# Kernel optimization log

Measured on AMD Instinct MI355X. Metric: run time of the kernel, lower is better.

Reference implementation:

```python
import jax, jax.numpy as jnp
import numpy as np

B, E, H, W, L = 16, 32, 512, 512, 3  # batch, emb channels, height, width, n classes (bg/plant/disease)
MAX_NEIGHBOR = 3


def _per_image_loss(emb, pred, label, neighbor):
    """emb: (E,H,W) f32; pred: (L,H,W) f32 logits; label: (H,W) int32; neighbor: (L,MAX_NEIGHBOR) int32."""
    P = H * W
    emb_f = emb.reshape(E, P)                                      # (E,P)
    lab_f = label.reshape(P)
    onehot = (lab_f[None, :] == jnp.arange(L)[:, None]).astype(emb.dtype)  # (L,P)
    counts = onehot.sum(axis=1)                                    # (L,)

    # per-label mean embeddings (segment mean) and L2-normalized means (F.normalize eps=1e-12)
    means = (onehot @ emb_f.T) / counts[:, None]                   # (L,E)
    norm_means = means / jnp.maximum(jnp.linalg.norm(means, axis=1, keepdims=True), 1e-12)

    # intra loss: mean over masked pixels of (1 - cos(norm_mean, pixel)), labels 1..L-1
    pix_hat = emb_f / jnp.maximum(jnp.linalg.norm(emb_f, axis=0, keepdims=True), 1e-8)  # CosineSimilarity eps
    cos = norm_means @ pix_hat                                     # (L,P)
    intra_per = (onehot * (1.0 - cos)).sum(axis=1) / counts        # (L,)
    intra = intra_per[1:].sum() / (L - 1)

    # inter loss: pairwise cosine of normalized means, masked by neighbor table
    S = norm_means @ norm_means.T                                  # (L,L)
    # inter_mask: for main_label>=1, mark neighbor entries until first 0 (break semantics)
    valid = jnp.cumprod((neighbor != 0).astype(jnp.float32), axis=1)        # (L,MAX_NEIGHBOR)
    rows = jnp.broadcast_to(jnp.arange(L)[:, None], (L, MAX_NEIGHBOR))
    row_ok = (rows >= 1).astype(jnp.float32)
    mask = jnp.zeros((L, L), dtype=jnp.float32).at[
        rows.reshape(-1), neighbor.reshape(-1)
    ].max((valid * row_ok).reshape(-1))
    inter = (S * mask).sum() / mask.sum()

    # cross-entropy (labels in [0,L), ignore_index=255 never hit here), mean over pixels
    logp = jax.nn.log_softmax(pred, axis=0)                        # (L,H,W)
    ce = -jnp.take_along_axis(logp, label[None, :, :].astype(jnp.int32), axis=0).mean()

    return intra + inter + ce


def setup_inputs() -> dict:
    key = jax.random.key(0)
    k1, k2, k3 = jax.random.split(key, 3)
    embedding = jax.random.normal(k1, (B, E, H, W), dtype=jnp.float32)
    prediction = jax.random.normal(k2, (B, L, H, W), dtype=jnp.float32)
    class_label = jax.random.randint(k3, (B, H, W), 0, L).astype(jnp.int32)
    # realistic neighbor table: plant(1)<->disease(2) adjacent, 0 = terminator
    nb = np.tile(np.array([[0, 0, 0], [2, 0, 0], [1, 0, 0]], dtype=np.int32), (B, 1, 1))
    neighbor = jnp.asarray(nb)
    return {"embedding": embedding, "prediction": prediction,
            "class_label": class_label, "neighbor": neighbor}


def reference(embedding, prediction, class_label, neighbor):
    losses = jax.vmap(_per_image_loss)(embedding, prediction, class_label, neighbor)  # (B,)
    return losses.sum()
```

## Files before the change

kernel.cpp:

```cpp
#include <hip/hip_runtime.h>
#include <math.h>

#define BATCH 16
#define EMB   32
#define HW    262144
#define NL    3

#define BLOCKS_PER_IMG 128
#define PX_PER_BLOCK  (HW / BLOCKS_PER_IMG)
#define TILE_PX       128
#define N_ITERS       (PX_PER_BLOCK / TILE_PX)

#define WS_COUNTS 0
#define WS_SE     64
#define WS_SH     (WS_SE + BATCH*96)
#define WS_CE     (WS_SH + BATCH*96)
#define WS_FLOATS (WS_CE + 1)

__device__ __forceinline__ float ce1(float a, float b, float c, int l) {
    const float m = fmaxf(fmaxf(a, b), c);
    const float s = __expf(a - m) + __expf(b - m) + __expf(c - m);
    const float zl = (l == 0) ? a : ((l == 1) ? b : c);
    return m + __logf(s) - zl;
}

__global__ __launch_bounds__(256) void fused_kernel(
        const float* __restrict__ emb, const float* __restrict__ pred,
        const int* __restrict__ label, float* __restrict__ ws)
{
    const int tid = threadIdx.x;
    const int ps  = tid & 31;
    const int eg  = tid >> 5;
    const int wv  = tid >> 6;
    const bool lowHalf = (tid & 63) < 32;
    const int b   = blockIdx.x / BLOCKS_PER_IMG;
    const int blk = blockIdx.x % BLOCKS_PER_IMG;

    const float* embB  = emb  + (size_t)b * EMB * HW;
    const float* predB = pred + (size_t)b * 3 * HW;
    const int*   labB  = label + (size_t)b * HW;
    const size_t pixBase = (size_t)blk * PX_PER_BLOCK;

    const float* ch0 = embB + (size_t)(eg*4+0)*HW;
    const float* ch1 = embB + (size_t)(eg*4+1)*HW;
    const float* ch2 = embB + (size_t)(eg*4+2)*HW;
    const float* ch3 = embB + (size_t)(eg*4+3)*HW;

    __shared__ float4 part[2][4][32];

    float accE[NL][4] = {};
    float accH[NL][4] = {};
    float cnt[NL] = {0.f, 0.f, 0.f};
    float ce = 0.f;

    size_t p = pixBase + (size_t)ps * 4;
    float4 v0 = *(const float4*)(ch0 + p);
    float4 v1 = *(const float4*)(ch1 + p);
    float4 v2 = *(const float4*)(ch2 + p);
    float4 v3 = *(const float4*)(ch3 + p);
    int4  lab = *(const int4*)(labB + p);

    for (int it = 0; it < N_ITERS; ++it) {
        const size_t pn = (it + 1 < N_ITERS) ? (p + TILE_PX)
                                             : (pixBase + (size_t)ps * 4);
        const float4 n0 = *(const float4*)(ch0 + pn);
        const float4 n1 = *(const float4*)(ch1 + pn);
        const float4 n2 = *(const float4*)(ch2 + pn);
        const float4 n3 = *(const float4*)(ch3 + pn);
        const int4 nlab = *(const int4*)(labB + pn);

        const bool doCE = (eg == (it & 7));
        float4 z0, z1, z2;
        if (doCE) {
            z0 = *(const float4*)(predB + p);
            z1 = *(const float4*)(predB + HW + p);
            z2 = *(const float4*)(predB + 2*HW + p);
        }

        float4 s;
        s.x = v0.x*v0.x + v1.x*v1.x + v2.x*v2.x + v3.x*v3.x;
        s.y = v0.y*v0.y + v1.y*v1.y + v2.y*v2.y + v3.y*v3.y;
        s.z = v0.z*v0.z + v1.z*v1.z + v2.z*v2.z + v3.z*v3.z;
        s.w = v0.w*v0.w + v1.w*v1.w + v2.w*v2.w + v3.w*v3.w;
        s.x += __shfl_xor(s.x, 32);
        s.y += __shfl_xor(s.y, 32);
        s.z += __shfl_xor(s.z, 32);
        s.w += __shfl_xor(s.w, 32);
        if (lowHalf) part[it & 1][wv][ps] = s;
        __syncthreads();
        const float4 t0 = part[it & 1][0][ps];
        const float4 t1 = part[it & 1][1][ps];
        const float4 t2 = part[it & 1][2][ps];
        const float4 t3 = part[it & 1][3][ps];
        float invn[4];
        invn[0] = 1.0f / fmaxf(sqrtf(t0.x + t1.x + t2.x + t3.x), 1e-8f);
        invn[1] = 1.0f / fmaxf(sqrtf(t0.y + t1.y + t2.y + t3.y), 1e-8f);
        invn[2] = 1.0f / fmaxf(sqrtf(t0.z + t1.z + t2.z + t3.z), 1e-8f);
        invn[3] = 1.0f / fmaxf(sqrtf(t0.w + t1.w + t2.w + t3.w), 1e-8f);

        const float chv[4][4] = {
            {v0.x, v1.x, v2.x, v3.x},
            {v0.y, v1.y, v2.y, v3.y},
            {v0.z, v1.z, v2.z, v3.z},
            {v0.w, v1.w, v2.w, v3.w}};
        const int labs[4] = {lab.x, lab.y, lab.z, lab.w};

        #pragma unroll
        for (int j = 0; j < 4; ++j) {
            const float m0 = (labs[j] == 0) ? 1.f : 0.f;
            const float m1 = (labs[j] == 1) ? 1.f : 0.f;
            const float m2 = (labs[j] == 2) ? 1.f : 0.f;
            const float iv = invn[j];
            if (eg == 0) { cnt[0] += m0; cnt[1] += m1; cnt[2] += m2; }
            #pragma unroll
            for (int k = 0; k < 4; ++k) {
                const float v  = chv[j][k];
                const float vh = v * iv;
                accE[0][k] = fmaf(m0, v,  accE[0][k]);
                accE[1][k] = fmaf(m1, v,  accE[1][k]);
                accE[2][k] = fmaf(m2, v,  accE[2][k]);
                accH[0][k] = fmaf(m0, vh, accH[0][k]);
                accH[1][k] = fmaf(m1, vh, accH[1][k]);
                accH[2][k] = fmaf(m2, vh, accH[2][k]);
            }
        }

        if (doCE) {
            ce += ce1(z0.x, z1.x, z2.x, labs[0]);
            ce += ce1(z0.y, z1.y, z2.y, labs[1]);
            ce += ce1(z0.z, z1.z, z2.z, labs[2]);
            ce += ce1(z0.w, z1.w, z2.w, labs[3]);
        }

        v0 = n0; v1 = n1; v2 = n2; v3 = n3; lab = nlab; p = pn;
    }

    #pragma unroll
    for (int o = 16; o >= 1; o >>= 1) {
        #pragma unroll
        for (int l = 0; l < NL; ++l) {
            #pragma unroll
            for (int k = 0; k < 4; ++k) {
                accE[l][k] += __shfl_xor(accE[l][k], o);
                accH[l][k] += __shfl_xor(accH[l][k], o);
            }
            cnt[l] += __shfl_xor(cnt[l], o);
        }
        ce += __shfl_xor(ce, o);
    }
    if (ps == 0) {
        float* se = ws + WS_SE + b * 96;
        float* sh = ws + WS_SH + b * 96;
        #pragma unroll
        for (int l = 0; l < NL; ++l) {
            #pragma unroll
            for (int k = 0; k < 4; ++k) {
                atomicAdd(&se[l*32 + eg*4 + k], accE[l][k]);
                atomicAdd(&sh[l*32 + eg*4 + k], accH[l][k]);
            }
        }
        atomicAdd(&ws[WS_CE], ce * (1.0f / (float)HW));
        if (eg == 0) {
            atomicAdd(&ws[WS_COUNTS + b*4 + 0], cnt[0]);
            atomicAdd(&ws[WS_COUNTS + b*4 + 1], cnt[1]);
            atomicAdd(&ws[WS_COUNTS + b*4 + 2], cnt[2]);
        }
    }
}

__global__ __launch_bounds__(512) void final_kernel(
        const int* __restrict__ nbr, const float* __restrict__ ws,
        float* __restrict__ out)
{
    const int tid = threadIdx.x;
    const int b = tid >> 5;
    const int e = tid & 31;
    __shared__ float total;
    if (tid == 0) total = 0.f;
    __syncthreads();

    const float* se = ws + WS_SE + b * 96;
    const float* sh = ws + WS_SH + b * 96;
    const float c0 = ws[WS_COUNTS + b*4 + 0];
    const float c1 = ws[WS_COUNTS + b*4 + 1];
    const float c2 = ws[WS_COUNTS + b*4 + 2];

    float mean0 = se[0*32 + e] / c0;
    float mean1 = se[1*32 + e] / c1;
    float mean2 = se[2*32 + e] / c2;

    float n0 = mean0*mean0, n1 = mean1*mean1, n2 = mean2*mean2;
    #pragma unroll
    for (int o = 16; o >= 1; o >>= 1) {
        n0 += __shfl_xor(n0, o);
        n1 += __shfl_xor(n1, o);
        n2 += __shfl_xor(n2, o);
    }
    const float nm0 = mean0 / fmaxf(sqrtf(n0), 1e-12f);
    const float nm1 = mean1 / fmaxf(sqrtf(n1), 1e-12f);
    const float nm2 = mean2 / fmaxf(sqrtf(n2), 1e-12f);

    float d1  = nm1 * sh[1*32 + e];
    float d2  = nm2 * sh[2*32 + e];
    float s10 = nm1 * nm0, s11 = nm1 * nm1, s12 = nm1 * nm2;
    float s20 = nm2 * nm0, s21 = nm2 * nm1, s22 = nm2 * nm2;
    #pragma unroll
    for (int o = 16; o >= 1; o >>= 1) {
        d1  += __shfl_xor(d1, o);  d2  += __shfl_xor(d2, o);
        s10 += __shfl_xor(s10, o); s11 += __shfl_xor(s11, o); s12 += __shfl_xor(s12, o);
        s20 += __shfl_xor(s20, o); s21 += __shfl_xor(s21, o); s22 += __shfl_xor(s22, o);
    }

    if (e == 0) {
        float S[3][3];
        S[1][0] = s10; S[1][1] = s11; S[1][2] = s12;
        S[2][0] = s20; S[2][1] = s21; S[2][2] = s22;
        S[0][0] = S[0][1] = S[0][2] = 0.f;
        float mask[3][3] = {{0.f,0.f,0.f},{0.f,0.f,0.f},{0.f,0.f,0.f}};
        for (int row = 1; row < 3; ++row) {
            int prod = 1;
            for (int j = 0; j < 3; ++j) {
                const int v = nbr[b*9 + row*3 + j];
                if (v == 0) prod = 0;
                if (prod) mask[row][v] = 1.f;
            }
        }
        float num = 0.f, den = 0.f;
        for (int row = 1; row < 3; ++row)
            for (int col = 0; col < 3; ++col) {
                num += S[row][col] * mask[row][col];
                den += mask[row][col];
            }
        const float inter = num / den;
        const float ip1 = 1.f - d1 / c1;
        const float ip2 = 1.f - d2 / c2;
        const float loss = 0.5f * (ip1 + ip2) + inter;
        atomicAdd(&total, loss);
    }
    __syncthreads();
    if (tid == 0) out[0] = total + ws[WS_CE];
}

extern "C" void kernel_launch(void* const* d_in, const int* in_sizes, int n_in,
                              void* d_out, int out_size, void* d_ws, size_t ws_size,
                              hipStream_t stream) {
    const float* emb   = (const float*)d_in[0];
    const float* pred  = (const float*)d_in[1];
    const int*   label = (const int*)d_in[2];
    const int*   nbr   = (const int*)d_in[3];
    float* ws  = (float*)d_ws;
    float* out = (float*)d_out;

    hipMemsetAsync(d_ws, 0, WS_FLOATS * sizeof(float), stream);
    fused_kernel<<<BATCH * BLOCKS_PER_IMG, 256, 0, stream>>>(emb, pred, label, ws);
    final_kernel<<<1, 512, 0, stream>>>(nbr, ws, out);
}
```

Before: 774.0 us.

## Map all channels of a pixel into one wave to drop block barriers

Each wave now holds all 32 channels for 32 pixels (8 pixel groups of 4 pixels by 8 channel groups), so the per-pixel norm is reduced with wave shuffles instead of shared memory and a per-iteration __syncthreads. Each wave handles its own pixel range. The explicit register prefetch of the next tile is removed. The unused label-0 normalized accumulator is also dropped, which cuts FMAs and atomics. In exchange, each load instruction now covers only 128 contiguous bytes per channel row, giving less coalescing per request, and losing the software prefetch may expose memory latency.

```diff
diff --git a/kernel.cpp b/kernel.cpp
--- a/kernel.cpp
+++ b/kernel.cpp
@@ -7,9 +7,11 @@
 #define NL    3
 
 #define BLOCKS_PER_IMG 128
-#define PX_PER_BLOCK  (HW / BLOCKS_PER_IMG)
-#define TILE_PX       128
-#define N_ITERS       (PX_PER_BLOCK / TILE_PX)
+#define PX_PER_BLOCK   (HW / BLOCKS_PER_IMG)
+#define WAVES_PER_BLK  4
+#define PX_PER_WAVE    (PX_PER_BLOCK / WAVES_PER_BLK)
+#define TILE_PX        32
+#define N_ITERS        (PX_PER_WAVE / TILE_PX)
 
 #define WS_COUNTS 0
 #define WS_SE     64
@@ -28,53 +30,49 @@
         const float* __restrict__ emb, const float* __restrict__ pred,
         const int* __restrict__ label, float* __restrict__ ws)
 {
-    const int tid = threadIdx.x;
-    const int ps  = tid & 31;
-    const int eg  = tid >> 5;
-    const int wv  = tid >> 6;
-    const bool lowHalf = (tid & 63) < 32;
-    const int b   = blockIdx.x / BLOCKS_PER_IMG;
-    const int blk = blockIdx.x % BLOCKS_PER_IMG;
-
-    const float* embB  = emb  + (size_t)b * EMB * HW;
-    const float* predB = pred + (size_t)b * 3 * HW;
+    const int tid  = threadIdx.x;
+    const int lane = tid & 63;
+    const int wv   = tid >> 6;
+    const int ps   = lane & 7;
+    const int cg   = lane >> 3;
+    const int b    = blockIdx.x / BLOCKS_PER_IMG;
+    const int blk  = blockIdx.x % BLOCKS_PER_IMG;
+
+    const float* embB  = emb   + (size_t)b * EMB * HW;
+    const float* predB = pred  + (size_t)b * 3 * HW;
     const int*   labB  = label + (size_t)b * HW;
-    const size_t pixBase = (size_t)blk * PX_PER_BLOCK;
-
-    const float* ch0 = embB + (size_t)(eg*4+0)*HW;
-    const float* ch1 = embB + (size_t)(eg*4+1)*HW;
-    const float* ch2 = embB + (size_t)(eg*4+2)*HW;
-    const float* ch3 = embB + (size_t)(eg*4+3)*HW;
-
-    __shared__ float4 part[2][4][32];
+
+    const size_t base = (size_t)blk * PX_PER_BLOCK
+                      + (size_t)wv * PX_PER_WAVE
+                      + (size_t)ps * 4;
+
+    const float* ch0 = embB + (size_t)(cg*4+0)*HW + base;
+    const float* ch1 = embB + (size_t)(cg*4+1)*HW + base;
+    const float* ch2 = embB + (size_t)(cg*4+2)*HW + base;
+    const float* ch3 = embB + (size_t)(cg*4+3)*HW + base;
+    const int*   lb  = labB + base;
+    const float* pr  = predB + base;
 
     float accE[NL][4] = {};
-    float accH[NL][4] = {};
-    float cnt[NL] = {0.f, 0.f, 0.f};
+    float accH[2][4]  = {};
+    float cnt0 = 0.f, cnt1 = 0.f, cnt2 = 0.f;
     float ce = 0.f;
 
-    size_t p = pixBase + (size_t)ps * 4;
-    float4 v0 = *(const float4*)(ch0 + p);
-    float4 v1 = *(const float4*)(ch1 + p);
-    float4 v2 = *(const float4*)(ch2 + p);
-    float4 v3 = *(const float4*)(ch3 + p);
-    int4  lab = *(const int4*)(labB + p);
-
     for (int it = 0; it < N_ITERS; ++it) {
-        const size_t pn = (it + 1 < N_ITERS) ? (p + TILE_PX)
-                                             : (pixBase + (size_t)ps * 4);
-        const float4 n0 = *(const float4*)(ch0 + pn);
-        const float4 n1 = *(const float4*)(ch1 + pn);
-        const float4 n2 = *(const float4*)(ch2 + pn);
-        const float4 n3 = *(const float4*)(ch3 + pn);
-        const int4 nlab = *(const int4*)(labB + pn);
-
-        const bool doCE = (eg == (it & 7));
+        const size_t off = (size_t)it * TILE_PX;
+
+        const float4 v0 = *(const float4*)(ch0 + off);
+        const float4 v1 = *(const float4*)(ch1 + off);
+        const float4 v2 = *(const float4*)(ch2 + off);
+        const float4 v3 = *(const float4*)(ch3 + off);
+        const int4  lab = *(const int4*)(lb + off);
+
+        const bool doCE = (cg == (it & 7));
         float4 z0, z1, z2;
         if (doCE) {
-            z0 = *(const float4*)(predB + p);
-            z1 = *(const float4*)(predB + HW + p);
-            z2 = *(const float4*)(predB + 2*HW + p);
+            z0 = *(const float4*)(pr + off);
+            z1 = *(const float4*)(pr + HW + off);
+            z2 = *(const float4*)(pr + 2*HW + off);
         }
 
         float4 s;
@@ -82,21 +80,16 @@
         s.y = v0.y*v0.y + v1.y*v1.y + v2.y*v2.y + v3.y*v3.y;
         s.z = v0.z*v0.z + v1.z*v1.z + v2.z*v2.z + v3.z*v3.z;
         s.w = v0.w*v0.w + v1.w*v1.w + v2.w*v2.w + v3.w*v3.w;
-        s.x += __shfl_xor(s.x, 32);
-        s.y += __shfl_xor(s.y, 32);
-        s.z += __shfl_xor(s.z, 32);
-        s.w += __shfl_xor(s.w, 32);
-        if (lowHalf) part[it & 1][wv][ps] = s;
-        __syncthreads();
-        const float4 t0 = part[it & 1][0][ps];
-        const float4 t1 = part[it & 1][1][ps];
-        const float4 t2 = part[it & 1][2][ps];
-        const float4 t3 = part[it & 1][3][ps];
+        s.x += __shfl_xor(s.x, 8);  s.x += __shfl_xor(s.x, 16);  s.x += __shfl_xor(s.x, 32);
+        s.y += __shfl_xor(s.y, 8);  s.y += __shfl_xor(s.y, 16);  s.y += __shfl_xor(s.y, 32);
+        s.z += __shfl_xor(s.z, 8);  s.z += __shfl_xor(s.z, 16);  s.z += __shfl_xor(s.z, 32);
+        s.w += __shfl_xor(s.w, 8);  s.w += __shfl_xor(s.w, 16);  s.w += __shfl_xor(s.w, 32);
+
         float invn[4];
-        invn[0] = 1.0f / fmaxf(sqrtf(t0.x + t1.x + t2.x + t3.x), 1e-8f);
-        invn[1] = 1.0f / fmaxf(sqrtf(t0.y + t1.y + t2.y + t3.y), 1e-8f);
-        invn[2] = 1.0f / fmaxf(sqrtf(t0.z + t1.z + t2.z + t3.z), 1e-8f);
-        invn[3] = 1.0f / fmaxf(sqrtf(t0.w + t1.w + t2.w + t3.w), 1e-8f);
+        invn[0] = 1.0f / fmaxf(sqrtf(s.x), 1e-8f);
+        invn[1] = 1.0f / fmaxf(sqrtf(s.y), 1e-8f);
+        invn[2] = 1.0f / fmaxf(sqrtf(s.z), 1e-8f);
+        invn[3] = 1.0f / fmaxf(sqrtf(s.w), 1e-8f);
 
         const float chv[4][4] = {
             {v0.x, v1.x, v2.x, v3.x},
@@ -111,7 +104,7 @@
             const float m1 = (labs[j] == 1) ? 1.f : 0.f;
             const float m2 = (labs[j] == 2) ? 1.f : 0.f;
             const float iv = invn[j];
-            if (eg == 0) { cnt[0] += m0; cnt[1] += m1; cnt[2] += m2; }
+            if (cg == 0) { cnt0 += m0; cnt1 += m1; cnt2 += m2; }
             #pragma unroll
             for (int k = 0; k < 4; ++k) {
                 const float v  = chv[j][k];
@@ -119,9 +112,8 @@
                 accE[0][k] = fmaf(m0, v,  accE[0][k]);
                 accE[1][k] = fmaf(m1, v,  accE[1][k]);
                 accE[2][k] = fmaf(m2, v,  accE[2][k]);
-                accH[0][k] = fmaf(m0, vh, accH[0][k]);
-                accH[1][k] = fmaf(m1, vh, accH[1][k]);
-                accH[2][k] = fmaf(m2, vh, accH[2][k]);
+                accH[0][k] = fmaf(m1, vh, accH[0][k]);
+                accH[1][k] = fmaf(m2, vh, accH[1][k]);
             }
         }
 
@@ -131,40 +123,46 @@
             ce += ce1(z0.z, z1.z, z2.z, labs[2]);
             ce += ce1(z0.w, z1.w, z2.w, labs[3]);
         }
-
-        v0 = n0; v1 = n1; v2 = n2; v3 = n3; lab = nlab; p = pn;
-    }
-
-    #pragma unroll
-    for (int o = 16; o >= 1; o >>= 1) {
-        #pragma unroll
-        for (int l = 0; l < NL; ++l) {
-            #pragma unroll
-            for (int k = 0; k < 4; ++k) {
+    }
+
+    #pragma unroll
+    for (int o = 4; o >= 1; o >>= 1) {
+        #pragma unroll
+        for (int l = 0; l < NL; ++l)
+            #pragma unroll
+            for (int k = 0; k < 4; ++k)
                 accE[l][k] += __shfl_xor(accE[l][k], o);
+        #pragma unroll
+        for (int l = 0; l < 2; ++l)
+            #pragma unroll
+            for (int k = 0; k < 4; ++k)
                 accH[l][k] += __shfl_xor(accH[l][k], o);
-            }
-            cnt[l] += __shfl_xor(cnt[l], o);
-        }
-        ce += __shfl_xor(ce, o);
-    }
+        cnt0 += __shfl_xor(cnt0, o);
+        cnt1 += __shfl_xor(cnt1, o);
+        cnt2 += __shfl_xor(cnt2, o);
+    }
+    #pragma unroll
+    for (int o = 32; o >= 1; o >>= 1) ce += __shfl_xor(ce, o);
+
     if (ps == 0) {
         float* se = ws + WS_SE + b * 96;
         float* sh = ws + WS_SH + b * 96;
         #pragma unroll
-        for (int l = 0; l < NL; ++l) {
-            #pragma unroll
-            for (int k = 0; k < 4; ++k) {
-                atomicAdd(&se[l*32 + eg*4 + k], accE[l][k]);
-                atomicAdd(&sh[l*32 + eg*4 + k], accH[l][k]);
-            }
-        }
+        for (int l = 0; l < NL; ++l)
+            #pragma unroll
+            for (int k = 0; k < 4; ++k)
+                atomicAdd(&se[l*32 + cg*4 + k], accE[l][k]);
+        #pragma unroll
+        for (int l = 0; l < 2; ++l)
+            #pragma unroll
+            for (int k = 0; k < 4; ++k)
+                atomicAdd(&sh[(l+1)*32 + cg*4 + k], accH[l][k]);
+    }
+    if (lane == 0) {
         atomicAdd(&ws[WS_CE], ce * (1.0f / (float)HW));
-        if (eg == 0) {
-            atomicAdd(&ws[WS_COUNTS + b*4 + 0], cnt[0]);
-            atomicAdd(&ws[WS_COUNTS + b*4 + 1], cnt[1]);
-            atomicAdd(&ws[WS_COUNTS + b*4 + 2], cnt[2]);
-        }
+        atomicAdd(&ws[WS_COUNTS + b*4 + 0], cnt0);
+        atomicAdd(&ws[WS_COUNTS + b*4 + 1], cnt1);
+        atomicAdd(&ws[WS_COUNTS + b*4 + 2], cnt2);
     }
 }
 
```

Result: slower. 864.7 us (+11.7%).
